# Optimization experiments

Hardware: AMD Instinct MI355X
Metric: run time of the kernel (lower is better)

The kernel has to match this reference:

```python
import jax, jax.numpy as jnp
import numpy as np


def _hardswish(x):
    return x * jnp.clip(x + 3.0, 0.0, 6.0) / 6.0


def _rel_coords_table(W):
    # [1, 2W-1, 2W-1, 2], log-spaced continuous relative coords (SwinV2)
    rc = jnp.arange(-(W - 1), W, dtype=jnp.float32)
    grid = jnp.stack(jnp.meshgrid(rc, rc, indexing='ij'), axis=-1)[None]
    grid = grid / float(W - 1) * 8.0
    return jnp.sign(grid) * jnp.log2(jnp.abs(grid) + 1.0) / np.float32(np.log2(8.0))


def _rel_pos_index(W):
    # [N, N] int indices into the (2W-1)^2 bias table
    coords = np.stack(np.meshgrid(np.arange(W), np.arange(W), indexing='ij')).reshape(2, -1)
    rel = (coords[:, :, None] - coords[:, None, :]).transpose(1, 2, 0)  # [N, N, 2]
    rel[:, :, 0] += W - 1
    rel[:, :, 1] += W - 1
    rel[:, :, 0] *= 2 * W - 1
    return jnp.asarray(rel.sum(-1))


def setup_inputs() -> dict:
    key = jax.random.key(0)
    ks = jax.random.split(key, 6)
    dim, num_heads, W = 512, 16, 8
    N = W * W
    B, nW = 2048, 64
    return {
        'x': jax.random.normal(ks[0], (B, N, dim), jnp.float32),
        'mask': jax.random.normal(ks[1], (nW, N, N), jnp.float32),
        'w_qkv': jax.random.normal(ks[2], (dim, 3 * dim), jnp.float32) * 0.02,
        'w_out': jax.random.normal(ks[3], (dim, dim), jnp.float32) * 0.02,
        'cpb_w1': jax.random.normal(ks[4], (2, 512), jnp.float32) * 0.02,
        'cpb_w2': jax.random.normal(ks[5], (512, num_heads), jnp.float32) * 0.02,
        'logits_scale': jnp.log(10.0 * jnp.ones((num_heads, 1, 1), jnp.float32)),
        'window_size': W,
        'num_heads': num_heads,
    }


def reference(x, mask, w_qkv, w_out, cpb_w1, cpb_w2, logits_scale, window_size, num_heads):
    B, N, C = x.shape
    hd = C // num_heads
    qkv = (x @ w_qkv).reshape(B, N, 3, num_heads, hd).transpose(2, 0, 3, 1, 4)
    q, k, v = qkv[0], qkv[1], qkv[2]  # [B, H, N, hd]

    # cosine attention (L2-normalized q, k) with clamped learned logit scale
    qn = q / jnp.clip(jnp.linalg.norm(q, axis=-1, keepdims=True), 1e-12)
    kn = k / jnp.clip(jnp.linalg.norm(k, axis=-1, keepdims=True), 1e-12)
    attn = jnp.einsum('bhnd,bhmd->bhnm', qn, kn)
    scale = jnp.exp(jnp.minimum(logits_scale, jnp.log(jnp.float32(100.0))))  # [H,1,1]
    attn = attn * scale[None]

    # continuous position bias via tiny MLP + index gather, sigmoid-scaled
    table = _rel_coords_table(window_size)                       # [1, 2W-1, 2W-1, 2]
    bias_table = (_hardswish(table @ cpb_w1) @ cpb_w2).reshape(-1, num_heads)
    idx = _rel_pos_index(window_size)                            # [N, N]
    bias = bias_table[idx.reshape(-1)].reshape(N, N, num_heads).transpose(2, 0, 1)
    attn = attn + 16.0 * jax.nn.sigmoid(bias)[None]

    if mask is not None:
        nW = mask.shape[0]
        attn = attn.reshape(B // nW, nW, num_heads, N, N) + mask[None, :, None]
        attn = attn.reshape(B, num_heads, N, N)

    # NOTE: original uses nn.Softmax(1) -> softmax over the HEAD axis; replicate faithfully
    attn = jax.nn.softmax(attn, axis=1)

    out = jnp.einsum('bhnm,bhmd->bhnd', attn, v).transpose(0, 2, 1, 3).reshape(B, N, C)
    return out @ w_out
```

## Files before the change

kernel.cpp:

```cpp
#include <hip/hip_runtime.h>
#include <hip/hip_bf16.h>

typedef unsigned short u16;
typedef unsigned int u32;
typedef __attribute__((ext_vector_type(8))) short bf16x8;
typedef __attribute__((ext_vector_type(4))) float f32x4;
typedef __attribute__((ext_vector_type(4))) float float4v;

__device__ __forceinline__ float bf2f(u16 v) {
  union { u32 u; float f; } x; x.u = ((u32)v) << 16; return x.f;
}
__device__ __forceinline__ u16 f2bf(float f) {
  union { u32 u; float f; } x; x.f = f;
  return (u16)((x.u + 0x7fffu + ((x.u >> 16) & 1u)) >> 16);
}

__device__ __forceinline__ void gload16(const void* g, void* l) {
  __builtin_amdgcn_global_load_lds(
      (const __attribute__((address_space(1))) u32*)g,
      (__attribute__((address_space(3))) u32*)l, 16, 0, 0);
}

#define MFMA16(a, bfr, cacc) __builtin_amdgcn_mfma_f32_16x16x32_bf16((a), (bfr), (cacc), 0, 0, 0)


__global__ void convert_bf16_kernel(const float* __restrict__ in,
                                    u16* __restrict__ out, int n8) {
  int t = blockIdx.x * blockDim.x + threadIdx.x;
  if (t >= n8) return;
  const float4v* p = (const float4v*)(in + (size_t)t * 8);
  float4v a = p[0], b = p[1];
  union { bf16x8 v; u16 s[8]; } o;
  o.s[0] = f2bf(a[0]); o.s[1] = f2bf(a[1]); o.s[2] = f2bf(a[2]); o.s[3] = f2bf(a[3]);
  o.s[4] = f2bf(b[0]); o.s[5] = f2bf(b[1]); o.s[6] = f2bf(b[2]); o.s[7] = f2bf(b[3]);
  *(bf16x8*)(out + (size_t)t * 8) = o.v;
}

__global__ void transpose_kernel(const float* __restrict__ in, u16* __restrict__ out,
                                 int R, int C) {
  int t = blockIdx.x * blockDim.x + threadIdx.x;
  if (t >= R * C) return;
  int c = t / R, r = t % R;
  out[t] = f2bf(in[r * C + c]);
}

__global__ void bias_tab_kernel(const float* __restrict__ w1, const float* __restrict__ w2,
                                float* __restrict__ tab) {
  int t = blockIdx.x * blockDim.x + threadIdx.x;
  if (t >= 225 * 16) return;
  int r = t >> 4, h = t & 15;
  int i = r / 15, j = r % 15;
  float gi = (float)(i - 7) * (8.0f / 7.0f);
  float gj = (float)(j - 7) * (8.0f / 7.0f);
  float si = (gi > 0.f) ? 1.f : ((gi < 0.f) ? -1.f : 0.f);
  float sj = (gj > 0.f) ? 1.f : ((gj < 0.f) ? -1.f : 0.f);
  float t0 = si * log2f(fabsf(gi) + 1.0f) * (1.0f / 3.0f);
  float t1 = sj * log2f(fabsf(gj) + 1.0f) * (1.0f / 3.0f);
  float acc = 0.f;
  for (int k = 0; k < 512; ++k) {
    float a = t0 * w1[k] + t1 * w1[512 + k];
    float hs = a * fminf(fmaxf(a + 3.f, 0.f), 6.f) * (1.f / 6.f);
    acc += hs * w2[k * 16 + h];
  }
  tab[t] = acc;
}

__global__ void bias16_kernel(const float* __restrict__ tab, float* __restrict__ b16) {
  int t = blockIdx.x * blockDim.x + threadIdx.x;
  if (t >= 16 * 64 * 64) return;
  int h = t >> 12, nm = t & 4095, n = nm >> 6, m = nm & 63;
  int idx = ((n >> 3) - (m >> 3) + 7) * 15 + ((n & 7) - (m & 7) + 7);
  float b = tab[idx * 16 + h];
  b16[t] = 16.0f / (1.0f + expf(-b));
}

template <bool F32OUT>
__global__ __launch_bounds__(256) void gemm_bt(const u16* __restrict__ A,
                                               const u16* __restrict__ Bt,
                                               void* __restrict__ Cout,
                                               int M, int N, int K) {
  __shared__ u16 lA[128 * 64];
  __shared__ u16 lB[128 * 64];
  const int tid = threadIdx.x;
  const int w = tid >> 6, l = tid & 63;
  const int lg = l >> 4, li = l & 15;
  const int nbn = N >> 7;
  const int nwg = gridDim.x;
  int bidx = blockIdx.x;
  int q = nwg >> 3, r = nwg & 7;
  int xcd = bidx & 7, pos = bidx >> 3;
  int swz = (xcd < r ? xcd * (q + 1) : r * (q + 1) + (xcd - r) * q) + pos;
  int bm = swz / nbn, bn = swz % nbn;
  const int wr = w >> 1, wc = w & 1;

  f32x4 acc[4][4];
#pragma unroll
  for (int i = 0; i < 4; i++)
#pragma unroll
    for (int j = 0; j < 4; j++) acc[i][j] = (f32x4){0.f, 0.f, 0.f, 0.f};

  const u16* Abase = A + (size_t)(bm * 128) * K;
  const u16* Bbase = Bt + (size_t)(bn * 128) * K;

  for (int k0 = 0; k0 < K; k0 += 64) {
#pragma unroll
    for (int i = 0; i < 4; ++i) {
      int c = w * 256 + i * 64 + l;
      int row = c >> 3, kc = c & 7;
      int kcs = kc ^ (row & 7);
      gload16(Abase + (size_t)row * K + k0 + kcs * 8, (u16*)lA + c * 8);
      gload16(Bbase + (size_t)row * K + k0 + kcs * 8, (u16*)lB + c * 8);
    }
    __syncthreads();
#pragma unroll
    for (int kk = 0; kk < 2; ++kk) {
      bf16x8 af[4], bfr[4];
#pragma unroll
      for (int t = 0; t < 4; ++t) {
        int row = wr * 64 + t * 16 + li;
        af[t] = *(const bf16x8*)&lA[row * 64 + (((kk * 4 + lg) ^ (row & 7)) << 3)];
        int col = wc * 64 + t * 16 + li;
        bfr[t] = *(const bf16x8*)&lB[col * 64 + (((kk * 4 + lg) ^ (col & 7)) << 3)];
      }
#pragma unroll
      for (int tm = 0; tm < 4; ++tm)
#pragma unroll
        for (int tn = 0; tn < 4; ++tn)
          acc[tm][tn] = MFMA16(af[tm], bfr[tn], acc[tm][tn]);
    }
    __syncthreads();
  }
  int r0 = bm * 128 + wr * 64 + lg * 4;
  int c0 = bn * 128 + wc * 64 + li;
#pragma unroll
  for (int tm = 0; tm < 4; ++tm)
#pragma unroll
    for (int tn = 0; tn < 4; ++tn)
#pragma unroll
      for (int j = 0; j < 4; ++j) {
        size_t off = (size_t)(r0 + tm * 16 + j) * N + c0 + tn * 16;
        if (F32OUT)
          ((float*)Cout)[off] = acc[tm][tn][j];
        else
          ((u16*)Cout)[off] = f2bf(acc[tm][tn][j]);
      }
}

__global__ __launch_bounds__(256) void gemm_qkv(const u16* __restrict__ A,
                                                const u16* __restrict__ Bt,
                                                u16* __restrict__ Cq,
                                                const float* __restrict__ lscale,
                                                int M, int K) {
  __shared__ u16 lds[128 * 136];
  u16* lA = lds;
  u16* lB = lds + 8192;
  const int tid = threadIdx.x;
  const int w = tid >> 6, l = tid & 63;
  const int lg = l >> 4, li = l & 15;
  const int nbn = 12;
  const int nwg = gridDim.x;
  int bidx = blockIdx.x;
  int q = nwg >> 3, r = nwg & 7;
  int xcd = bidx & 7, pos = bidx >> 3;
  int swz = (xcd < r ? xcd * (q + 1) : r * (q + 1) + (xcd - r) * q) + pos;
  int bm = swz / nbn, bn = swz % nbn;
  const int wr = w >> 1, wc = w & 1;

  f32x4 acc[4][4];
#pragma unroll
  for (int i = 0; i < 4; i++)
#pragma unroll
    for (int j = 0; j < 4; j++) acc[i][j] = (f32x4){0.f, 0.f, 0.f, 0.f};

  const u16* Abase = A + (size_t)(bm * 128) * K;
  const u16* Bbase = Bt + (size_t)(bn * 128) * K;

  for (int k0 = 0; k0 < K; k0 += 64) {
#pragma unroll
    for (int i = 0; i < 4; ++i) {
      int c = w * 256 + i * 64 + l;
      int row = c >> 3, kc = c & 7;
      int kcs = kc ^ (row & 7);
      gload16(Abase + (size_t)row * K + k0 + kcs * 8, lA + c * 8);
      gload16(Bbase + (size_t)row * K + k0 + kcs * 8, lB + c * 8);
    }
    __syncthreads();
#pragma unroll
    for (int kk = 0; kk < 2; ++kk) {
      bf16x8 af[4], bfr[4];
#pragma unroll
      for (int t = 0; t < 4; ++t) {
        int row = wr * 64 + t * 16 + li;
        af[t] = *(const bf16x8*)&lA[row * 64 + (((kk * 4 + lg) ^ (row & 7)) << 3)];
        int col = wc * 64 + t * 16 + li;
        bfr[t] = *(const bf16x8*)&lB[col * 64 + (((kk * 4 + lg) ^ (col & 7)) << 3)];
      }
#pragma unroll
      for (int tm = 0; tm < 4; ++tm)
#pragma unroll
        for (int tn = 0; tn < 4; ++tn)
          acc[tm][tn] = MFMA16(af[tm], bfr[tn], acc[tm][tn]);
    }
    __syncthreads();
  }

  const int s_t = bn >> 2;
  const int hq = (bn & 3) * 4;
  if (s_t < 2) {
    float scv[2];
    if (s_t == 0) {
      scv[0] = __expf(fminf(lscale[hq + wc * 2 + 0], 4.6051702f));
      scv[1] = __expf(fminf(lscale[hq + wc * 2 + 1], 4.6051702f));
    } else {
      scv[0] = scv[1] = 1.0f;
    }
#pragma unroll
    for (int tm = 0; tm < 4; ++tm)
#pragma unroll
      for (int g = 0; g < 2; ++g) {
        f32x4 s2;
#pragma unroll
        for (int j = 0; j < 4; ++j)
          s2[j] = acc[tm][2 * g][j] * acc[tm][2 * g][j] +
                  acc[tm][2 * g + 1][j] * acc[tm][2 * g + 1][j];
#pragma unroll
        for (int m = 1; m <= 8; m <<= 1)
#pragma unroll
          for (int j = 0; j < 4; ++j) s2[j] += __shfl_xor(s2[j], m);
#pragma unroll
        for (int j = 0; j < 4; ++j) {
          float rn = scv[g] / fmaxf(sqrtf(s2[j]), 1e-12f);
          acc[tm][2 * g][j] *= rn;
          acc[tm][2 * g + 1][j] *= rn;
        }
      }
    u16* ct = lds;
#pragma unroll
    for (int tm = 0; tm < 4; ++tm)
#pragma unroll
      for (int tn = 0; tn < 4; ++tn)
#pragma unroll
        for (int j = 0; j < 4; ++j)
          ct[(wr * 64 + tm * 16 + lg * 4 + j) * 136 + wc * 64 + tn * 16 + li] =
              f2bf(acc[tm][tn][j]);
    __syncthreads();
    {
      int rr = tid >> 2;
      int c8 = (tid & 3) * 8;
#pragma unroll
      for (int bh = 0; bh < 2; ++bh)
#pragma unroll
        for (int ht = 0; ht < 4; ++ht) {
          bf16x8 v = *(const bf16x8*)(ct + (bh * 64 + rr) * 136 + ht * 32 + c8);
          size_t base = ((size_t)(s_t * 16 + hq + ht) * 2048 + (bm * 2 + bh)) * 2048;
          *(bf16x8*)(Cq + base + rr * 32 + c8) = v;
        }
    }
  } else {
    u16* ctT = lds;
#pragma unroll
    for (int tm = 0; tm < 4; ++tm)
#pragma unroll
      for (int tn = 0; tn < 4; ++tn)
#pragma unroll
        for (int j = 0; j < 4; ++j)
          ctT[(wc * 64 + tn * 16 + li) * 136 + wr * 64 + tm * 16 + lg * 4 + j] =
              f2bf(acc[tm][tn][j]);
    __syncthreads();
#pragma unroll
    for (int r2 = 0; r2 < 8; ++r2) {
      int id = r2 * 256 + tid;
      int colc = id >> 4;
      int seg = id & 15;
      bf16x8 v = *(const bf16x8*)&ctT[colc * 136 + seg * 8];
      int ht = colc >> 5, d = colc & 31;
      int wi = seg >> 3, n0 = (seg & 7) * 8;
      size_t base = ((size_t)(32 + hq + ht) * 2048 + (bm * 2 + wi)) * 2048;
      *(bf16x8*)(Cq + base + d * 64 + n0) = v;
    }
  }
}

__global__ __launch_bounds__(512, 2) void attn2(const u16* __restrict__ qkv,
                                                const float* __restrict__ mask,
                                                const float* __restrict__ bias16,
                                                u16* __restrict__ aout) {
  __shared__ float S[16 * 16 * 65];
  u16* P16 = (u16*)S;
  float* ob = S;
  const int tid = threadIdx.x;
  const int w = tid >> 6, l = tid & 63;
  const int lg = l >> 4, li = l & 15;
  const int b = blockIdx.x, wm = b & 63;
  const float* mask_w = mask + wm * 4096;

  bf16x8 qfr[2][4];
#pragma unroll
  for (int hp = 0; hp < 2; ++hp) {
    const u16* qb = qkv + ((size_t)(w + hp * 8) * 2048 + b) * 2048;
#pragma unroll
    for (int tn = 0; tn < 4; ++tn)
      qfr[hp][tn] = *(const bf16x8*)(qb + (tn * 16 + li) * 32 + lg * 8);
  }

  f32x4 oacc[2][4][2];
#pragma unroll
  for (int hp = 0; hp < 2; ++hp)
#pragma unroll
    for (int i = 0; i < 4; ++i) {
      oacc[hp][i][0] = (f32x4){0.f, 0.f, 0.f, 0.f};
      oacc[hp][i][1] = (f32x4){0.f, 0.f, 0.f, 0.f};
    }

#pragma unroll
  for (int c = 0; c < 4; ++c) {
#pragma unroll
    for (int hp = 0; hp < 2; ++hp) {
      int h = w + hp * 8;
      const u16* kb = qkv + ((size_t)(16 + h) * 2048 + b) * 2048;
      const float* bias_h = bias16 + h * 4096;
      bf16x8 kfc = *(const bf16x8*)(kb + (c * 16 + li) * 32 + lg * 8);
      int mg = c * 16 + li;
#pragma unroll
      for (int tn = 0; tn < 4; ++tn) {
        f32x4 z = {0.f, 0.f, 0.f, 0.f};
        f32x4 s = MFMA16(qfr[hp][tn], kfc, z);
#pragma unroll
        for (int j = 0; j < 4; ++j) {
          int n = tn * 16 + lg * 4 + j;
          S[h * 1040 + li * 65 + n] = s[j] + bias_h[n * 64 + mg] + mask_w[n * 64 + mg];
        }
      }
    }
    __syncthreads();
#pragma unroll
    for (int pp = 0; pp < 2; ++pp) {
      int p = tid + pp * 512;
      int base = (p >> 6) * 65 + (p & 63);
      float vals[16];
      float mx = -3.0e38f;
#pragma unroll
      for (int hh = 0; hh < 16; ++hh) {
        vals[hh] = S[hh * 1040 + base];
        mx = fmaxf(mx, vals[hh]);
      }
      float sum = 0.f;
#pragma unroll
      for (int hh = 0; hh < 16; ++hh) {
        float e = __expf(vals[hh] - mx);
        vals[hh] = e;
        sum += e;
      }
      float inv = 1.0f / sum;
#pragma unroll
      for (int hh = 0; hh < 16; ++hh)
        P16[(hh * 1040 + base) * 2] = f2bf(vals[hh] * inv);
    }
    __syncthreads();
#pragma unroll
    for (int hp = 0; hp < 2; ++hp) {
      int h = w + hp * 8;
      const u16* vbT = qkv + ((size_t)(32 + h) * 2048 + b) * 2048;
      bf16x8 vf[2];
      if (lg < 2) {
#pragma unroll
        for (int td = 0; td < 2; ++td)
          vf[td] = *(const bf16x8*)(vbT + (td * 16 + li) * 64 + c * 16 + lg * 8);
      } else {
#pragma unroll
        for (int td = 0; td < 2; ++td)
#pragma unroll
          for (int e = 0; e < 8; ++e) vf[td][e] = 0;
      }
#pragma unroll
      for (int tn = 0; tn < 4; ++tn) {
        bf16x8 pf;
#pragma unroll
        for (int e = 0; e < 8; ++e)
          pf[e] = (lg < 2)
                      ? (short)P16[(h * 1040 + (lg * 8 + e) * 65 + tn * 16 + li) * 2]
                      : (short)0;
        oacc[hp][tn][0] = MFMA16(pf, vf[0], oacc[hp][tn][0]);
        oacc[hp][tn][1] = MFMA16(pf, vf[1], oacc[hp][tn][1]);
      }
    }
    __syncthreads();
  }

#pragma unroll
  for (int tn = 0; tn < 4; ++tn) {
#pragma unroll
    for (int hp = 0; hp < 2; ++hp) {
      int h = w + hp * 8;
#pragma unroll
      for (int td = 0; td < 2; ++td)
#pragma unroll
        for (int j = 0; j < 4; ++j)
          ob[(lg * 4 + j) * 516 + h * 32 + td * 16 + li] = oacc[hp][tn][td][j];
    }
    __syncthreads();
    {
      int rr = tid >> 5, c16 = (tid & 31) * 16;
      const float* src = ob + rr * 516 + c16;
      u16* dst = aout + ((size_t)b * 64 + tn * 16 + rr) * 512 + c16;
#pragma unroll
      for (int half = 0; half < 2; ++half) {
        union { bf16x8 v; u16 u[8]; } o;
#pragma unroll
        for (int e = 0; e < 8; ++e) o.u[e] = f2bf(src[half * 8 + e]);
        *(bf16x8*)(dst + half * 8) = o.v;
      }
    }
    __syncthreads();
  }
}

extern "C" void kernel_launch(void* const* d_in, const int* in_sizes, int n_in,
                              void* d_out, int out_size, void* d_ws, size_t ws_size,
                              hipStream_t stream) {
  const float* x = (const float*)d_in[0];
  const float* mask = (const float*)d_in[1];
  const float* w_qkv = (const float*)d_in[2];
  const float* w_out = (const float*)d_in[3];
  const float* cpb_w1 = (const float*)d_in[4];
  const float* cpb_w2 = (const float*)d_in[5];
  const float* lscale = (const float*)d_in[6];
  float* out = (float*)d_out;

  char* ws = (char*)d_ws;
  u16* wqkvT = (u16*)ws;
  u16* woutT = (u16*)(ws + 1572864ull);
  float* btab = (float*)(ws + 2097152ull);
  float* b16 = (float*)(ws + 2113536ull);
  u16* qkv_ws = (u16*)(ws + 2375680ull);
  u16* xb = (u16*)(ws + 2375680ull + 402653184ull);
  u16* attn_out = xb;

  transpose_kernel<<<(512 * 1536 + 255) / 256, 256, 0, stream>>>(w_qkv, wqkvT, 512, 1536);
  transpose_kernel<<<(512 * 512 + 255) / 256, 256, 0, stream>>>(w_out, woutT, 512, 512);
  bias_tab_kernel<<<(225 * 16 + 255) / 256, 256, 0, stream>>>(cpb_w1, cpb_w2, btab);
  bias16_kernel<<<(16 * 64 * 64 + 255) / 256, 256, 0, stream>>>(btab, b16);

  convert_bf16_kernel<<<(131072 * 64 + 255) / 256, 256, 0, stream>>>(x, xb, 131072 * 64);

  gemm_qkv<<<12288, 256, 0, stream>>>(xb, wqkvT, qkv_ws, lscale, 131072, 512);

  attn2<<<2048, 512, 0, stream>>>(qkv_ws, mask, b16, attn_out);

  gemm_bt<true><<<4096, 256, 0, stream>>>(attn_out, woutT, out, 131072, 512, 512);
}
```

Before: 961.6 us.

## Fuse output projection into attention kernel and split QKV GEMM into QK and V

The output projection GEMM is folded into the attention kernel's epilogue. The per-window attention output is staged as bf16 in shared memory and multiplied by the transposed w_out, with B fragments read directly from global memory, and fp32 results are written straight to the output. This removes the bf16 round-trip of the attention output through HBM and one kernel launch. The QKV GEMM is also split into two specialized kernels (QK with normalization, V with a transposed store) to remove a divergent epilogue branch. The risks are extra register pressure and uncached global reads of w_out inside the occupancy-limited attention kernel.

```diff
diff --git a/kernel.cpp b/kernel.cpp
--- a/kernel.cpp
+++ b/kernel.cpp
@@ -74,17 +74,18 @@
   b16[t] = 16.0f / (1.0f + expf(-b));
 }
 
-template <bool F32OUT>
-__global__ __launch_bounds__(256) void gemm_bt(const u16* __restrict__ A,
+__global__ __launch_bounds__(256) void gemm_qk(const u16* __restrict__ A,
                                                const u16* __restrict__ Bt,
-                                               void* __restrict__ Cout,
-                                               int M, int N, int K) {
-  __shared__ u16 lA[128 * 64];
-  __shared__ u16 lB[128 * 64];
+                                               u16* __restrict__ Cq,
+                                               const float* __restrict__ lscale,
+                                               int M, int K) {
+  __shared__ u16 lds[128 * 136];
+  u16* lA = lds;
+  u16* lB = lds + 8192;
   const int tid = threadIdx.x;
   const int w = tid >> 6, l = tid & 63;
   const int lg = l >> 4, li = l & 15;
-  const int nbn = N >> 7;
+  const int nbn = 8;
   const int nwg = gridDim.x;
   int bidx = blockIdx.x;
   int q = nwg >> 3, r = nwg & 7;
@@ -108,8 +109,8 @@
       int c = w * 256 + i * 64 + l;
       int row = c >> 3, kc = c & 7;
       int kcs = kc ^ (row & 7);
-      gload16(Abase + (size_t)row * K + k0 + kcs * 8, (u16*)lA + c * 8);
-      gload16(Bbase + (size_t)row * K + k0 + kcs * 8, (u16*)lB + c * 8);
+      gload16(Abase + (size_t)row * K + k0 + kcs * 8, lA + c * 8);
+      gload16(Bbase + (size_t)row * K + k0 + kcs * 8, lB + c * 8);
     }
     __syncthreads();
 #pragma unroll
@@ -130,34 +131,71 @@
     }
     __syncthreads();
   }
-  int r0 = bm * 128 + wr * 64 + lg * 4;
-  int c0 = bn * 128 + wc * 64 + li;
+
+  const int s_t = bn >> 2;
+  const int hq = (bn & 3) * 4;
+  float scv[2];
+  if (s_t == 0) {
+    scv[0] = __expf(fminf(lscale[hq + wc * 2 + 0], 4.6051702f));
+    scv[1] = __expf(fminf(lscale[hq + wc * 2 + 1], 4.6051702f));
+  } else {
+    scv[0] = scv[1] = 1.0f;
+  }
 #pragma unroll
   for (int tm = 0; tm < 4; ++tm)
 #pragma unroll
+    for (int g = 0; g < 2; ++g) {
+      f32x4 s2;
+#pragma unroll
+      for (int j = 0; j < 4; ++j)
+        s2[j] = acc[tm][2 * g][j] * acc[tm][2 * g][j] +
+                acc[tm][2 * g + 1][j] * acc[tm][2 * g + 1][j];
+#pragma unroll
+      for (int m = 1; m <= 8; m <<= 1)
+#pragma unroll
+        for (int j = 0; j < 4; ++j) s2[j] += __shfl_xor(s2[j], m);
+#pragma unroll
+      for (int j = 0; j < 4; ++j) {
+        float rn = scv[g] / fmaxf(sqrtf(s2[j]), 1e-12f);
+        acc[tm][2 * g][j] *= rn;
+        acc[tm][2 * g + 1][j] *= rn;
+      }
+    }
+  u16* ct = lds;
+#pragma unroll
+  for (int tm = 0; tm < 4; ++tm)
+#pragma unroll
     for (int tn = 0; tn < 4; ++tn)
 #pragma unroll
-      for (int j = 0; j < 4; ++j) {
-        size_t off = (size_t)(r0 + tm * 16 + j) * N + c0 + tn * 16;
-        if (F32OUT)
-          ((float*)Cout)[off] = acc[tm][tn][j];
-        else
-          ((u16*)Cout)[off] = f2bf(acc[tm][tn][j]);
-      }
-}
-
-__global__ __launch_bounds__(256) void gemm_qkv(const u16* __restrict__ A,
-                                                const u16* __restrict__ Bt,
-                                                u16* __restrict__ Cq,
-                                                const float* __restrict__ lscale,
-                                                int M, int K) {
+      for (int j = 0; j < 4; ++j)
+        ct[(wr * 64 + tm * 16 + lg * 4 + j) * 136 + wc * 64 + tn * 16 + li] =
+            f2bf(acc[tm][tn][j]);
+  __syncthreads();
+  {
+    int rr = tid >> 2;
+    int c8 = (tid & 3) * 8;
+#pragma unroll
+    for (int bh = 0; bh < 2; ++bh)
+#pragma unroll
+      for (int ht = 0; ht < 4; ++ht) {
+        bf16x8 v = *(const bf16x8*)(ct + (bh * 64 + rr) * 136 + ht * 32 + c8);
+        size_t base = ((size_t)(s_t * 16 + hq + ht) * 2048 + (bm * 2 + bh)) * 2048;
+        *(bf16x8*)(Cq + base + rr * 32 + c8) = v;
+      }
+  }
+}
+
+__global__ __launch_bounds__(256) void gemm_v(const u16* __restrict__ A,
+                                              const u16* __restrict__ Bt,
+                                              u16* __restrict__ Cq,
+                                              int M, int K) {
   __shared__ u16 lds[128 * 136];
   u16* lA = lds;
   u16* lB = lds + 8192;
   const int tid = threadIdx.x;
   const int w = tid >> 6, l = tid & 63;
   const int lg = l >> 4, li = l & 15;
-  const int nbn = 12;
+  const int nbn = 4;
   const int nwg = gridDim.x;
   int bidx = blockIdx.x;
   int q = nwg >> 3, r = nwg & 7;
@@ -204,90 +242,38 @@
     __syncthreads();
   }
 
-  const int s_t = bn >> 2;
-  const int hq = (bn & 3) * 4;
-  if (s_t < 2) {
-    float scv[2];
-    if (s_t == 0) {
-      scv[0] = __expf(fminf(lscale[hq + wc * 2 + 0], 4.6051702f));
-      scv[1] = __expf(fminf(lscale[hq + wc * 2 + 1], 4.6051702f));
-    } else {
-      scv[0] = scv[1] = 1.0f;
-    }
-#pragma unroll
-    for (int tm = 0; tm < 4; ++tm)
-#pragma unroll
-      for (int g = 0; g < 2; ++g) {
-        f32x4 s2;
-#pragma unroll
-        for (int j = 0; j < 4; ++j)
-          s2[j] = acc[tm][2 * g][j] * acc[tm][2 * g][j] +
-                  acc[tm][2 * g + 1][j] * acc[tm][2 * g + 1][j];
-#pragma unroll
-        for (int m = 1; m <= 8; m <<= 1)
-#pragma unroll
-          for (int j = 0; j < 4; ++j) s2[j] += __shfl_xor(s2[j], m);
-#pragma unroll
-        for (int j = 0; j < 4; ++j) {
-          float rn = scv[g] / fmaxf(sqrtf(s2[j]), 1e-12f);
-          acc[tm][2 * g][j] *= rn;
-          acc[tm][2 * g + 1][j] *= rn;
-        }
-      }
-    u16* ct = lds;
-#pragma unroll
-    for (int tm = 0; tm < 4; ++tm)
-#pragma unroll
-      for (int tn = 0; tn < 4; ++tn)
-#pragma unroll
-        for (int j = 0; j < 4; ++j)
-          ct[(wr * 64 + tm * 16 + lg * 4 + j) * 136 + wc * 64 + tn * 16 + li] =
-              f2bf(acc[tm][tn][j]);
-    __syncthreads();
-    {
-      int rr = tid >> 2;
-      int c8 = (tid & 3) * 8;
-#pragma unroll
-      for (int bh = 0; bh < 2; ++bh)
-#pragma unroll
-        for (int ht = 0; ht < 4; ++ht) {
-          bf16x8 v = *(const bf16x8*)(ct + (bh * 64 + rr) * 136 + ht * 32 + c8);
-          size_t base = ((size_t)(s_t * 16 + hq + ht) * 2048 + (bm * 2 + bh)) * 2048;
-          *(bf16x8*)(Cq + base + rr * 32 + c8) = v;
-        }
-    }
-  } else {
-    u16* ctT = lds;
-#pragma unroll
-    for (int tm = 0; tm < 4; ++tm)
-#pragma unroll
-      for (int tn = 0; tn < 4; ++tn)
-#pragma unroll
-        for (int j = 0; j < 4; ++j)
-          ctT[(wc * 64 + tn * 16 + li) * 136 + wr * 64 + tm * 16 + lg * 4 + j] =
-              f2bf(acc[tm][tn][j]);
-    __syncthreads();
-#pragma unroll
-    for (int r2 = 0; r2 < 8; ++r2) {
-      int id = r2 * 256 + tid;
-      int colc = id >> 4;
-      int seg = id & 15;
-      bf16x8 v = *(const bf16x8*)&ctT[colc * 136 + seg * 8];
-      int ht = colc >> 5, d = colc & 31;
-      int wi = seg >> 3, n0 = (seg & 7) * 8;
-      size_t base = ((size_t)(32 + hq + ht) * 2048 + (bm * 2 + wi)) * 2048;
-      *(bf16x8*)(Cq + base + d * 64 + n0) = v;
-    }
+  const int hq = bn * 4;
+  u16* ctT = lds;
+#pragma unroll
+  for (int tm = 0; tm < 4; ++tm)
+#pragma unroll
+    for (int tn = 0; tn < 4; ++tn)
+#pragma unroll
+      for (int j = 0; j < 4; ++j)
+        ctT[(wc * 64 + tn * 16 + li) * 136 + wr * 64 + tm * 16 + lg * 4 + j] =
+            f2bf(acc[tm][tn][j]);
+  __syncthreads();
+#pragma unroll
+  for (int r2 = 0; r2 < 8; ++r2) {
+    int id = r2 * 256 + tid;
+    int colc = id >> 4;
+    int seg = id & 15;
+    bf16x8 v = *(const bf16x8*)&ctT[colc * 136 + seg * 8];
+    int ht = colc >> 5, d = colc & 31;
+    int wi = seg >> 3, n0 = (seg & 7) * 8;
+    size_t base = ((size_t)(32 + hq + ht) * 2048 + (bm * 2 + wi)) * 2048;
+    *(bf16x8*)(Cq + base + d * 64 + n0) = v;
   }
 }
 
 __global__ __launch_bounds__(512, 2) void attn2(const u16* __restrict__ qkv,
                                                 const float* __restrict__ mask,
                                                 const float* __restrict__ bias16,
-                                                u16* __restrict__ aout) {
-  __shared__ float S[16 * 16 * 65];
+                                                const u16* __restrict__ woT,
+                                                float* __restrict__ outp) {
+  __shared__ float S[16704];
   u16* P16 = (u16*)S;
-  float* ob = S;
+  u16* o16 = (u16*)S;
   const int tid = threadIdx.x;
   const int w = tid >> 6, l = tid & 63;
   const int lg = l >> 4, li = l & 15;
@@ -388,30 +374,50 @@
   }
 
 #pragma unroll
-  for (int tn = 0; tn < 4; ++tn) {
-#pragma unroll
-    for (int hp = 0; hp < 2; ++hp) {
-      int h = w + hp * 8;
+  for (int tn = 0; tn < 4; ++tn)
+#pragma unroll
+    for (int hp = 0; hp < 2; ++hp)
 #pragma unroll
       for (int td = 0; td < 2; ++td)
 #pragma unroll
         for (int j = 0; j < 4; ++j)
-          ob[(lg * 4 + j) * 516 + h * 32 + td * 16 + li] = oacc[hp][tn][td][j];
-    }
-    __syncthreads();
-    {
-      int rr = tid >> 5, c16 = (tid & 31) * 16;
-      const float* src = ob + rr * 516 + c16;
-      u16* dst = aout + ((size_t)b * 64 + tn * 16 + rr) * 512 + c16;
-#pragma unroll
-      for (int half = 0; half < 2; ++half) {
-        union { bf16x8 v; u16 u[8]; } o;
-#pragma unroll
-        for (int e = 0; e < 8; ++e) o.u[e] = f2bf(src[half * 8 + e]);
-        *(bf16x8*)(dst + half * 8) = o.v;
-      }
-    }
-    __syncthreads();
+          o16[(tn * 16 + lg * 4 + j) * 522 + (w + hp * 8) * 32 + td * 16 + li] =
+              f2bf(oacc[hp][tn][td][j]);
+  __syncthreads();
+#pragma unroll
+  for (int p = 0; p < 2; ++p) {
+    f32x4 acc2[4][2];
+#pragma unroll
+    for (int i = 0; i < 4; ++i) {
+      acc2[i][0] = (f32x4){0.f, 0.f, 0.f, 0.f};
+      acc2[i][1] = (f32x4){0.f, 0.f, 0.f, 0.f};
+    }
+#pragma unroll
+    for (int kk = 0; kk < 16; ++kk) {
+      bf16x8 af[4];
+#pragma unroll
+      for (int t = 0; t < 4; ++t)
+        af[t] = *(const bf16x8*)&o16[(t * 16 + li) * 522 + kk * 32 + lg * 8];
+      bf16x8 bf2[2];
+#pragma unroll
+      for (int tn = 0; tn < 2; ++tn)
+        bf2[tn] = *(const bf16x8*)(woT +
+                                   (size_t)(w * 64 + p * 32 + tn * 16 + li) * 512 +
+                                   kk * 32 + lg * 8);
+#pragma unroll
+      for (int tm = 0; tm < 4; ++tm)
+#pragma unroll
+        for (int tn = 0; tn < 2; ++tn)
+          acc2[tm][tn] = MFMA16(af[tm], bf2[tn], acc2[tm][tn]);
+    }
+#pragma unroll
+    for (int tm = 0; tm < 4; ++tm)
+#pragma unroll
+      for (int tn = 0; tn < 2; ++tn)
+#pragma unroll
+        for (int j = 0; j < 4; ++j)
+          outp[((size_t)b * 64 + tm * 16 + lg * 4 + j) * 512 +
+               w * 64 + p * 32 + tn * 16 + li] = acc2[tm][tn][j];
   }
 }
 
@@ -434,7 +440,6 @@
   float* b16 = (float*)(ws + 2113536ull);
   u16* qkv_ws = (u16*)(ws + 2375680ull);
   u16* xb = (u16*)(ws + 2375680ull + 402653184ull);
-  u16* attn_out = xb;
 
   transpose_kernel<<<(512 * 1536 + 255) / 256, 256, 0, stream>>>(w_qkv, wqkvT, 512, 1536);
   transpose_kernel<<<(512 * 512 + 255) / 256, 256, 0, stream>>>(w_out, woutT, 512, 512);
@@ -443,9 +448,8 @@
 
   convert_bf16_kernel<<<(131072 * 64 + 255) / 256, 256, 0, stream>>>(x, xb, 131072 * 64);
 
-  gemm_qkv<<<12288, 256, 0, stream>>>(xb, wqkvT, qkv_ws, lscale, 131072, 512);
-
-  attn2<<<2048, 512, 0, stream>>>(qkv_ws, mask, b16, attn_out);
-
-  gemm_bt<true><<<4096, 256, 0, stream>>>(attn_out, woutT, out, 131072, 512, 512);
-}
+  gemm_qk<<<8192, 256, 0, stream>>>(xb, wqkvT, qkv_ws, lscale, 131072, 512);
+  gemm_v<<<4096, 256, 0, stream>>>(xb, wqkvT + (size_t)1024 * 512, qkv_ws, 131072, 512);
+
+  attn2<<<2048, 512, 0, stream>>>(qkv_ws, mask, b16, woutT, out);
+}
```

Result: slower. 1.010 ms (+5.1%).
